# Performance work log

Hardware: AMD Instinct MI355X
Metric: run time of the kernel (lower is better)

## Reference

```python
import jax, jax.numpy as jnp
import numpy as np

EMB, KEY, HEAD, CTX = 1024, 64, 64, 4096
B, T = 4, 4096

def setup_inputs() -> dict:
    key = jax.random.key(0)
    ks = jax.random.split(key, 4)
    s = 1.0 / np.sqrt(EMB)
    return {
        "embeddings": jax.random.normal(ks[0], (B, T, EMB), dtype=jnp.float32),
        "Wk": jax.random.normal(ks[1], (EMB, KEY), dtype=jnp.float32) * s,
        "bk": jnp.zeros((KEY,), dtype=jnp.float32),
        "Wq": jax.random.normal(ks[2], (EMB, KEY), dtype=jnp.float32) * s,
        "bq": jnp.zeros((KEY,), dtype=jnp.float32),
        "Wv": jax.random.normal(ks[3], (EMB, HEAD), dtype=jnp.float32) * s,
        "bv": jnp.zeros((HEAD,), dtype=jnp.float32),
    }

def reference(embeddings, Wk, bk, Wq, bq, Wv, bv):
    # Linear projections: [B, T, E] @ [E, D] -> [B, T, D]
    keys = embeddings @ Wk + bk
    queries = embeddings @ Wq + bq
    values = embeddings @ Wv + bv
    # Scores: [B, T, T]
    scores = jnp.einsum("btd,bsd->bts", queries, keys) / jnp.sqrt(jnp.float32(KEY))
    t = scores.shape[1]
    # causal mask: -inf strictly above diagonal
    causal = jnp.tril(jnp.ones((t, t), dtype=bool))
    scores = jnp.where(causal, scores, -jnp.inf)
    weights = jax.nn.softmax(scores, axis=-1)
    return jnp.einsum("bts,bsh->bth", weights, values)
```

## Files before the change

### kernel.cpp

```cpp
#include <hip/hip_runtime.h>
#include <hip/hip_bf16.h>

#define EMB 1024
#define NB  4
#define TT  4096
#define DD  64

static constexpr float SCALE2 = 0.125f * 1.4426950408889634f;

typedef __bf16          bfrag    __attribute__((ext_vector_type(8)));
typedef float           f32x4    __attribute__((ext_vector_type(4)));
typedef unsigned short  ushort8t __attribute__((ext_vector_type(8)));
typedef unsigned short  ushort4t __attribute__((ext_vector_type(4)));
typedef unsigned int    uint32;

__device__ __forceinline__ unsigned short f2bf(float f) {
    __hip_bfloat16 h = __float2bfloat16(f);
    return __builtin_bit_cast(unsigned short, h);
}
__device__ __forceinline__ float bf2f(unsigned short u) {
    uint32 v = ((uint32)u) << 16;
    return __builtin_bit_cast(float, v);
}
__device__ __forceinline__ uint32 pk2(float a, float b) {
    return (uint32)f2bf(a) | ((uint32)f2bf(b) << 16);
}

__global__ __launch_bounds__(256) void prep_wt(
    const float* __restrict__ Wk, const float* __restrict__ Wq,
    const float* __restrict__ Wv, unsigned short* __restrict__ Wt)
{
    const int o = blockIdx.x * 256 + threadIdx.x;
    const int n = o >> 10, k = o & 1023;
    float v;
    if (n < 64)       v = Wk[k * 64 + n];
    else if (n < 128) v = Wq[k * 64 + (n - 64)] * SCALE2;
    else              v = Wv[k * 64 + (n - 128)];
    Wt[o] = f2bf(v);
}

#define PSTR 66

__global__ __launch_bounds__(256) void qkv_mfma(
    const float* __restrict__ emb,
    const unsigned short* __restrict__ Wt,
    const float* __restrict__ bk, const float* __restrict__ bq,
    const float* __restrict__ bv,
    unsigned short* __restrict__ Qb, unsigned short* __restrict__ Kb,
    unsigned short* __restrict__ Vt)
{
    __shared__ unsigned short elds[64 * PSTR];
    __shared__ unsigned short wlds[192 * PSTR];

    const int tid = threadIdx.x;
    const int w = tid >> 6, l = tid & 63;
    const int lr = l & 15, lg = l >> 4;
    const int m0 = blockIdx.x * 64;

    f32x4 acc[12];
#pragma unroll
    for (int i = 0; i < 12; ++i) acc[i] = (f32x4){0.f, 0.f, 0.f, 0.f};

    const int er = tid >> 2, ec = (tid & 3) * 16;

    float4 f0, f1, f2, f3;
    ushort8t wr[6];
    {
        const float* src = emb + (size_t)(m0 + er) * EMB + ec;
        f0 = *(const float4*)(src + 0);
        f1 = *(const float4*)(src + 4);
        f2 = *(const float4*)(src + 8);
        f3 = *(const float4*)(src + 12);
#pragma unroll
        for (int i = 0; i < 6; ++i) {
            const int idx = tid + i * 256;
            const int row = idx >> 3, c = (idx & 7) * 8;
            wr[i] = *(const ushort8t*)&Wt[(size_t)row * 1024 + c];
        }
    }

    for (int it = 0; it < 16; ++it) {
        __syncthreads();
        {
            ushort8t lo, hi;
            lo[0]=f2bf(f0.x); lo[1]=f2bf(f0.y); lo[2]=f2bf(f0.z); lo[3]=f2bf(f0.w);
            lo[4]=f2bf(f1.x); lo[5]=f2bf(f1.y); lo[6]=f2bf(f1.z); lo[7]=f2bf(f1.w);
            hi[0]=f2bf(f2.x); hi[1]=f2bf(f2.y); hi[2]=f2bf(f2.z); hi[3]=f2bf(f2.w);
            hi[4]=f2bf(f3.x); hi[5]=f2bf(f3.y); hi[6]=f2bf(f3.z); hi[7]=f2bf(f3.w);
            *(ushort8t*)&elds[er * PSTR + ec]     = lo;
            *(ushort8t*)&elds[er * PSTR + ec + 8] = hi;
#pragma unroll
            for (int i = 0; i < 6; ++i) {
                const int idx = tid + i * 256;
                const int row = idx >> 3, c = (idx & 7) * 8;
                *(ushort8t*)&wlds[row * PSTR + c] = wr[i];
            }
        }
        if (it < 15) {
            const int kn = (it + 1) * 64;
            const float* src = emb + (size_t)(m0 + er) * EMB + kn + ec;
            f0 = *(const float4*)(src + 0);
            f1 = *(const float4*)(src + 4);
            f2 = *(const float4*)(src + 8);
            f3 = *(const float4*)(src + 12);
#pragma unroll
            for (int i = 0; i < 6; ++i) {
                const int idx = tid + i * 256;
                const int row = idx >> 3, c = (idx & 7) * 8;
                wr[i] = *(const ushort8t*)&Wt[(size_t)row * 1024 + kn + c];
            }
        }
        __syncthreads();
#pragma unroll
        for (int c = 0; c < 2; ++c) {
            bfrag a = *(const bfrag*)&elds[(w * 16 + lr) * PSTR + c * 32 + lg * 8];
#pragma unroll
            for (int nt = 0; nt < 12; ++nt) {
                bfrag bb = *(const bfrag*)&wlds[(nt * 16 + lr) * PSTR + c * 32 + lg * 8];
                acc[nt] = __builtin_amdgcn_mfma_f32_16x16x32_bf16(a, bb, acc[nt], 0, 0, 0);
            }
        }
    }

    const int rbase = m0 + w * 16 + lg * 4;
#pragma unroll
    for (int nt = 0; nt < 12; ++nt) {
        const int n = nt * 16 + lr;
        float bias;
        if (n < 64)       bias = bk[n];
        else if (n < 128) bias = bq[n - 64] * SCALE2;
        else              bias = bv[n - 128];
        if (nt < 8) {
            unsigned short* dst = (nt < 4) ? Kb : Qb;
            const int d = (nt < 4) ? n : (n - 64);
#pragma unroll
            for (int rg = 0; rg < 4; ++rg)
                dst[(size_t)(rbase + rg) * 64 + d] = f2bf(acc[nt][rg] + bias);
        } else {
            const int h = n - 128;
            const int b = rbase >> 12, t = rbase & (TT - 1);
            ushort4t pk;
#pragma unroll
            for (int rg = 0; rg < 4; ++rg) pk[rg] = f2bf(acc[nt][rg] + bias);
            *(ushort4t*)&Vt[((size_t)b * 64 + h) * TT + t] = pk;
        }
    }
}

#define PST 66

__global__ __launch_bounds__(64) void attn_part(
    const unsigned short* __restrict__ Qb,
    const unsigned short* __restrict__ Kb,
    const unsigned short* __restrict__ Vt,
    unsigned short* __restrict__ po, float* __restrict__ pml,
    int chunk, int nch)
{
    __shared__ unsigned short plds[32 * PST];

    const int idx  = blockIdx.x;
    const int c    = idx >> 9;
    const int b    = idx & 3;
    const int ti32 = 127 - ((idx >> 2) & 127);
    const int nkt  = (ti32 >> 1) + 1;
    const int kt0  = c * chunk;
    if (kt0 >= nkt) return;
    const int kt1 = min(nkt, kt0 + chunk);

    const int l  = threadIdx.x;
    const int lr = l & 15, g = l >> 4;
    const int q0 = ti32 * 32;
    const size_t bTT = (size_t)b * TT;

    bfrag qa[2][2];
#pragma unroll
    for (int s = 0; s < 2; ++s) {
        const size_t qr = (bTT + q0 + s * 16 + lr) * 64 + g * 8;
        qa[s][0] = *(const bfrag*)&Qb[qr];
        qa[s][1] = *(const bfrag*)&Qb[qr + 32];
    }

    f32x4 o[2][4];
#pragma unroll
    for (int s = 0; s < 2; ++s)
#pragma unroll
        for (int ht = 0; ht < 4; ++ht) o[s][ht] = (f32x4){0.f, 0.f, 0.f, 0.f};
    float mrow[2] = {-1e30f, -1e30f};
    float lrow[2] = {0.f, 0.f};

    for (int kt = kt0; kt < kt1; ++kt) {
        const int k0 = kt * 64;

        bfrag kf[4][2];
#pragma unroll
        for (int nt = 0; nt < 4; ++nt) {
            const size_t kr = (bTT + k0 + nt * 16 + lr) * 64 + g * 8;
            kf[nt][0] = *(const bfrag*)&Kb[kr];
            kf[nt][1] = *(const bfrag*)&Kb[kr + 32];
        }
        bfrag vf[4][2];
#pragma unroll
        for (int ht = 0; ht < 4; ++ht) {
            const size_t vr = ((size_t)b * 64 + ht * 16 + lr) * TT + k0 + g * 8;
            vf[ht][0] = *(const bfrag*)&Vt[vr];
            vf[ht][1] = *(const bfrag*)&Vt[vr + 32];
        }
        const bool diag = (kt == nkt - 1);

#pragma unroll
        for (int s = 0; s < 2; ++s) {
            f32x4 sv[4];
#pragma unroll
            for (int nt = 0; nt < 4; ++nt) {
                sv[nt] = (f32x4){0.f, 0.f, 0.f, 0.f};
                sv[nt] = __builtin_amdgcn_mfma_f32_16x16x32_bf16(kf[nt][0], qa[s][0], sv[nt], 0, 0, 0);
                sv[nt] = __builtin_amdgcn_mfma_f32_16x16x32_bf16(kf[nt][1], qa[s][1], sv[nt], 0, 0, 0);
            }
            const int qrow = q0 + s * 16 + lr;
            if (diag) {
#pragma unroll
                for (int nt = 0; nt < 4; ++nt)
#pragma unroll
                    for (int rg = 0; rg < 4; ++rg) {
                        const int key = k0 + nt * 16 + 4 * g + rg;
                        if (key > qrow) sv[nt][rg] = -1e30f;
                    }
            }
            float pm = sv[0][0];
#pragma unroll
            for (int nt = 0; nt < 4; ++nt)
#pragma unroll
                for (int rg = 0; rg < 4; ++rg) pm = fmaxf(pm, sv[nt][rg]);
            pm = fmaxf(pm, __shfl_xor(pm, 16));
            pm = fmaxf(pm, __shfl_xor(pm, 32));

            if (!__all(pm - mrow[s] <= 8.0f)) {
                const float nm = fmaxf(mrow[s], pm);
                const float cr = exp2f(mrow[s] - nm);
                mrow[s] = nm;
                lrow[s] *= cr;
#pragma unroll
                for (int ht = 0; ht < 4; ++ht) o[s][ht] *= cr;
            }

            float ls = 0.f;
            uint32 pw[8];
#pragma unroll
            for (int nt = 0; nt < 4; ++nt)
#pragma unroll
                for (int h = 0; h < 2; ++h) {
                    const float pa_ = exp2f(sv[nt][2 * h]     - mrow[s]);
                    const float pb_ = exp2f(sv[nt][2 * h + 1] - mrow[s]);
                    ls += pa_ + pb_;
                    pw[nt * 2 + h] = pk2(pa_, pb_);
                }
            ls += __shfl_xor(ls, 16);
            ls += __shfl_xor(ls, 32);
            lrow[s] += ls;

            const int prow = (s * 16 + lr) * PST;
#pragma unroll
            for (int nt = 0; nt < 4; ++nt)
#pragma unroll
                for (int h = 0; h < 2; ++h)
                    *(uint32*)&plds[prow + nt * 16 + 4 * g + 2 * h] = pw[nt * 2 + h];

#pragma unroll
            for (int cc = 0; cc < 2; ++cc) {
                bfrag pa = *(const bfrag*)&plds[prow + cc * 32 + g * 8];
#pragma unroll
                for (int ht = 0; ht < 4; ++ht)
                    o[s][ht] = __builtin_amdgcn_mfma_f32_16x16x32_bf16(pa, vf[ht][cc], o[s][ht], 0, 0, 0);
            }
        }
    }

    const int slot = (((b << 7) + ti32) * nch) + c;
    const size_t pob = (size_t)slot * 2048;
#pragma unroll
    for (int s = 0; s < 2; ++s)
#pragma unroll
        for (int ht = 0; ht < 4; ++ht)
#pragma unroll
            for (int rg = 0; rg < 4; ++rg)
                po[pob + (size_t)(((s * 4 + ht) * 4 + rg) * 64 + l)] = f2bf(o[s][ht][rg]);
    if (g == 0) {
#pragma unroll
        for (int s = 0; s < 2; ++s) {
            pml[slot * 64 + s * 16 + lr]      = mrow[s];
            pml[slot * 64 + 32 + s * 16 + lr] = lrow[s];
        }
    }
}

__global__ __launch_bounds__(256) void attn_merge(
    const unsigned short* __restrict__ po, const float* __restrict__ pml,
    float* __restrict__ out, int chunk, int nch)
{
    const int idx  = blockIdx.x;
    const int b    = idx & 3;
    const int ti32 = idx >> 2;
    const int nkt  = (ti32 >> 1) + 1;
    const int nc   = (nkt + chunk - 1) / chunk;

    const int e0   = threadIdx.x * 8;
    const int lane = e0 & 63;
    const int rg   = (e0 >> 6) & 3;
    const int ht   = (e0 >> 8) & 3;
    const int s    = e0 >> 10;
    const int row  = s * 16 + ((lane >> 4) << 2) + rg;
    const int col0 = ht * 16 + (lane & 15);
    const int slot0 = ((b << 7) + ti32) * nch;

    float M = -1e30f;
    for (int c = 0; c < nc; ++c)
        M = fmaxf(M, pml[(slot0 + c) * 64 + row]);

    float den = 0.f;
    float acc[8];
#pragma unroll
    for (int i = 0; i < 8; ++i) acc[i] = 0.f;

    for (int c = 0; c < nc; ++c) {
        const float wgt = exp2f(pml[(slot0 + c) * 64 + row] - M);
        den += wgt * pml[(slot0 + c) * 64 + 32 + row];
        const ushort8t v = *(const ushort8t*)&po[(size_t)(slot0 + c) * 2048 + e0];
#pragma unroll
        for (int j = 0; j < 8; ++j) acc[j] += wgt * bf2f(v[j]);
    }
    const float inv = 1.0f / den;
    float* dst = out + ((size_t)b * TT + ti32 * 32 + row) * 64 + col0;
    float4 o0 = {acc[0] * inv, acc[1] * inv, acc[2] * inv, acc[3] * inv};
    float4 o1 = {acc[4] * inv, acc[5] * inv, acc[6] * inv, acc[7] * inv};
    *(float4*)(dst)     = o0;
    *(float4*)(dst + 4) = o1;
}

extern "C" void kernel_launch(void* const* d_in, const int* in_sizes, int n_in,
                              void* d_out, int out_size, void* d_ws, size_t ws_size,
                              hipStream_t stream)
{
    const float* emb = (const float*)d_in[0];
    const float* Wk  = (const float*)d_in[1];
    const float* bk  = (const float*)d_in[2];
    const float* Wq  = (const float*)d_in[3];
    const float* bq  = (const float*)d_in[4];
    const float* Wv  = (const float*)d_in[5];
    const float* bv  = (const float*)d_in[6];
    float* out = (float*)d_out;

    char* base = (char*)d_ws;
    unsigned short* Qb = (unsigned short*)(base);
    unsigned short* Kb = (unsigned short*)(base + (2u << 20));
    unsigned short* Vt = (unsigned short*)(base + (4u << 20));
    unsigned short* Wt = (unsigned short*)(base + (6u << 20));
    const size_t pbase = ((size_t)6 << 20) + (512u << 10);

    int nch = 8;
    for (;;) {
        const size_t need = pbase +
            (size_t)512 * nch * (2048 * sizeof(unsigned short) + 64 * sizeof(float));
        if (need <= ws_size || nch == 1) break;
        nch >>= 1;
    }
    const int chunk = 64 / nch;
    unsigned short* po = (unsigned short*)(base + pbase);
    float* pml = (float*)(po + (size_t)512 * nch * 2048);

    prep_wt<<<192 * 1024 / 256, 256, 0, stream>>>(Wk, Wq, Wv, Wt);
    qkv_mfma<<<(NB * TT) / 64, 256, 0, stream>>>(emb, Wt, bk, bq, bv, Qb, Kb, Vt);
    attn_part<<<512 * nch, 64, 0, stream>>>(Qb, Kb, Vt, po, pml, chunk, nch);
    attn_merge<<<512, 256, 0, stream>>>(po, pml, out, chunk, nch);
}
```

Measured before the change: 85.85 us.

## Double-buffer K loads, permute P in registers, and retune QKV and split counts

The attention partial kernel now double-buffers K fragments across key tiles and loads V ahead of compute. It replaces the LDS round-trip for the probability matrix with ds_bpermute register shuffles and raises MFMA priority with s_setprio. The key-split count goes from 8 to 16 chunks through a templated chunk size, when workspace allows. The QKV projection kernel moves to 32-row tiles with 128 threads, doubling its block count. Together these aim to hide global load latency and raise occupancy, at the cost of more registers, more partial results to merge, and more redundant weight-tile loads in the projection.

```diff
diff --git a/kernel.cpp b/kernel.cpp
--- a/kernel.cpp
+++ b/kernel.cpp
@@ -13,6 +13,7 @@
 typedef unsigned short  ushort8t __attribute__((ext_vector_type(8)));
 typedef unsigned short  ushort4t __attribute__((ext_vector_type(4)));
 typedef unsigned int    uint32;
+typedef uint32          uint32x4 __attribute__((ext_vector_type(4)));
 
 __device__ __forceinline__ unsigned short f2bf(float f) {
     __hip_bfloat16 h = __float2bfloat16(f);
@@ -41,7 +42,7 @@
 
 #define PSTR 66
 
-__global__ __launch_bounds__(256) void qkv_mfma(
+__global__ __launch_bounds__(128) void qkv_mfma(
     const float* __restrict__ emb,
     const unsigned short* __restrict__ Wt,
     const float* __restrict__ bk, const float* __restrict__ bq,
@@ -49,13 +50,13 @@
     unsigned short* __restrict__ Qb, unsigned short* __restrict__ Kb,
     unsigned short* __restrict__ Vt)
 {
-    __shared__ unsigned short elds[64 * PSTR];
+    __shared__ unsigned short elds[32 * PSTR];
     __shared__ unsigned short wlds[192 * PSTR];
 
     const int tid = threadIdx.x;
     const int w = tid >> 6, l = tid & 63;
     const int lr = l & 15, lg = l >> 4;
-    const int m0 = blockIdx.x * 64;
+    const int m0 = blockIdx.x * 32;
 
     f32x4 acc[12];
 #pragma unroll
@@ -64,7 +65,7 @@
     const int er = tid >> 2, ec = (tid & 3) * 16;
 
     float4 f0, f1, f2, f3;
-    ushort8t wr[6];
+    ushort8t wr[12];
     {
         const float* src = emb + (size_t)(m0 + er) * EMB + ec;
         f0 = *(const float4*)(src + 0);
@@ -72,8 +73,8 @@
         f2 = *(const float4*)(src + 8);
         f3 = *(const float4*)(src + 12);
 #pragma unroll
-        for (int i = 0; i < 6; ++i) {
-            const int idx = tid + i * 256;
+        for (int i = 0; i < 12; ++i) {
+            const int idx = tid + i * 128;
             const int row = idx >> 3, c = (idx & 7) * 8;
             wr[i] = *(const ushort8t*)&Wt[(size_t)row * 1024 + c];
         }
@@ -90,8 +91,8 @@
             *(ushort8t*)&elds[er * PSTR + ec]     = lo;
             *(ushort8t*)&elds[er * PSTR + ec + 8] = hi;
 #pragma unroll
-            for (int i = 0; i < 6; ++i) {
-                const int idx = tid + i * 256;
+            for (int i = 0; i < 12; ++i) {
+                const int idx = tid + i * 128;
                 const int row = idx >> 3, c = (idx & 7) * 8;
                 *(ushort8t*)&wlds[row * PSTR + c] = wr[i];
             }
@@ -104,8 +105,8 @@
             f2 = *(const float4*)(src + 8);
             f3 = *(const float4*)(src + 12);
 #pragma unroll
-            for (int i = 0; i < 6; ++i) {
-                const int idx = tid + i * 256;
+            for (int i = 0; i < 12; ++i) {
+                const int idx = tid + i * 128;
                 const int row = idx >> 3, c = (idx & 7) * 8;
                 wr[i] = *(const ushort8t*)&Wt[(size_t)row * 1024 + kn + c];
             }
@@ -147,25 +148,113 @@
     }
 }
 
-#define PST 66
-
-__global__ __launch_bounds__(64) void attn_part(
+#define LOADK(KF, T)                                                          \
+    { const unsigned short* p_ = kp0 + (size_t)(T) * 4096;                    \
+      KF[0][0] = *(const bfrag*)(p_);         KF[0][1] = *(const bfrag*)(p_ + 32);   \
+      KF[1][0] = *(const bfrag*)(p_ + 1024);  KF[1][1] = *(const bfrag*)(p_ + 1056); \
+      KF[2][0] = *(const bfrag*)(p_ + 2048);  KF[2][1] = *(const bfrag*)(p_ + 2080); \
+      KF[3][0] = *(const bfrag*)(p_ + 3072);  KF[3][1] = *(const bfrag*)(p_ + 3104); }
+
+#define LOADV(VF, T)                                                          \
+    { const unsigned short* p_ = vp0 + (T) * 64;                              \
+      VF[0][0] = *(const bfrag*)(p_);             VF[0][1] = *(const bfrag*)(p_ + 32);           \
+      VF[1][0] = *(const bfrag*)(p_ + 16 * TT);   VF[1][1] = *(const bfrag*)(p_ + 16 * TT + 32); \
+      VF[2][0] = *(const bfrag*)(p_ + 32 * TT);   VF[2][1] = *(const bfrag*)(p_ + 32 * TT + 32); \
+      VF[3][0] = *(const bfrag*)(p_ + 48 * TT);   VF[3][1] = *(const bfrag*)(p_ + 48 * TT + 32); }
+
+#define COMPUTE(KF, VF, T)                                                    \
+{                                                                             \
+    const int  kt_   = kt0 + (T);                                             \
+    const bool diag_ = (kt_ == nkt - 1);                                      \
+    const int  k0_   = kt_ * 64;                                              \
+    _Pragma("unroll")                                                         \
+    for (int s = 0; s < 2; ++s) {                                             \
+        f32x4 sv[4];                                                          \
+        __builtin_amdgcn_s_setprio(1);                                        \
+        _Pragma("unroll")                                                     \
+        for (int nt = 0; nt < 4; ++nt) {                                      \
+            sv[nt] = (f32x4){0.f, 0.f, 0.f, 0.f};                             \
+            sv[nt] = __builtin_amdgcn_mfma_f32_16x16x32_bf16(KF[nt][0], qa[s][0], sv[nt], 0, 0, 0); \
+            sv[nt] = __builtin_amdgcn_mfma_f32_16x16x32_bf16(KF[nt][1], qa[s][1], sv[nt], 0, 0, 0); \
+        }                                                                     \
+        __builtin_amdgcn_s_setprio(0);                                        \
+        const int qrow_ = q0 + s * 16 + lr;                                   \
+        if (diag_) {                                                          \
+            _Pragma("unroll")                                                 \
+            for (int nt = 0; nt < 4; ++nt)                                    \
+                _Pragma("unroll")                                             \
+                for (int rg = 0; rg < 4; ++rg) {                              \
+                    const int key_ = k0_ + nt * 16 + 4 * g + rg;              \
+                    if (key_ > qrow_) sv[nt][rg] = -1e30f;                    \
+                }                                                             \
+        }                                                                     \
+        float pm = fmaxf(fmaxf(fmaxf(sv[0][0], sv[0][1]), fmaxf(sv[0][2], sv[0][3])),   \
+                         fmaxf(fmaxf(sv[1][0], sv[1][1]), fmaxf(sv[1][2], sv[1][3])));  \
+        pm = fmaxf(pm, fmaxf(fmaxf(fmaxf(sv[2][0], sv[2][1]), fmaxf(sv[2][2], sv[2][3])),   \
+                             fmaxf(fmaxf(sv[3][0], sv[3][1]), fmaxf(sv[3][2], sv[3][3])))); \
+        pm = fmaxf(pm, __shfl_xor(pm, 16));                                   \
+        pm = fmaxf(pm, __shfl_xor(pm, 32));                                   \
+        if (!__all(pm - mrow[s] <= 8.0f)) {                                   \
+            const float nm_ = fmaxf(mrow[s], pm);                             \
+            const float cr_ = exp2f(mrow[s] - nm_);                           \
+            mrow[s] = nm_;                                                    \
+            lrow[s] *= cr_;                                                   \
+            _Pragma("unroll")                                                 \
+            for (int ht = 0; ht < 4; ++ht) o[s][ht] *= cr_;                   \
+        }                                                                     \
+        float ls = 0.f;                                                       \
+        uint32 pw[8];                                                         \
+        _Pragma("unroll")                                                     \
+        for (int nt = 0; nt < 4; ++nt)                                        \
+            _Pragma("unroll")                                                 \
+            for (int h = 0; h < 2; ++h) {                                     \
+                const float pa_ = exp2f(sv[nt][2 * h]     - mrow[s]);         \
+                const float pb_ = exp2f(sv[nt][2 * h + 1] - mrow[s]);         \
+                ls += pa_ + pb_;                                              \
+                pw[nt * 2 + h] = pk2(pa_, pb_);                               \
+            }                                                                 \
+        ls += __shfl_xor(ls, 16);                                             \
+        ls += __shfl_xor(ls, 32);                                             \
+        lrow[s] += ls;                                                        \
+        _Pragma("unroll")                                                     \
+        for (int cc = 0; cc < 2; ++cc) {                                      \
+            uint32x4 dw;                                                      \
+            _Pragma("unroll")                                                 \
+            for (int w2 = 0; w2 < 4; ++w2) {                                  \
+                const int addr_ = (w2 < 2) ? addr_a : addr_b;                 \
+                const uint32 lo_ = (uint32)__builtin_amdgcn_ds_bpermute(      \
+                    addr_, (int)pw[4 * cc + (w2 & 1)]);                       \
+                const uint32 hi_ = (uint32)__builtin_amdgcn_ds_bpermute(      \
+                    addr_, (int)pw[4 * cc + 2 + (w2 & 1)]);                   \
+                dw[w2] = ghi ? hi_ : lo_;                                     \
+            }                                                                 \
+            const bfrag paf_ = __builtin_bit_cast(bfrag, dw);                 \
+            __builtin_amdgcn_s_setprio(1);                                    \
+            o[s][0] = __builtin_amdgcn_mfma_f32_16x16x32_bf16(paf_, VF[0][cc], o[s][0], 0, 0, 0); \
+            o[s][1] = __builtin_amdgcn_mfma_f32_16x16x32_bf16(paf_, VF[1][cc], o[s][1], 0, 0, 0); \
+            o[s][2] = __builtin_amdgcn_mfma_f32_16x16x32_bf16(paf_, VF[2][cc], o[s][2], 0, 0, 0); \
+            o[s][3] = __builtin_amdgcn_mfma_f32_16x16x32_bf16(paf_, VF[3][cc], o[s][3], 0, 0, 0); \
+            __builtin_amdgcn_s_setprio(0);                                    \
+        }                                                                     \
+    }                                                                         \
+}
+
+template<int CHUNK>
+__global__ __launch_bounds__(64, 2) void attn_part(
     const unsigned short* __restrict__ Qb,
     const unsigned short* __restrict__ Kb,
     const unsigned short* __restrict__ Vt,
-    unsigned short* __restrict__ po, float* __restrict__ pml,
-    int chunk, int nch)
+    unsigned short* __restrict__ po, float* __restrict__ pml)
 {
-    __shared__ unsigned short plds[32 * PST];
-
+    constexpr int NCH = 64 / CHUNK;
     const int idx  = blockIdx.x;
     const int c    = idx >> 9;
     const int b    = idx & 3;
     const int ti32 = 127 - ((idx >> 2) & 127);
     const int nkt  = (ti32 >> 1) + 1;
-    const int kt0  = c * chunk;
+    const int kt0  = c * CHUNK;
     if (kt0 >= nkt) return;
-    const int kt1 = min(nkt, kt0 + chunk);
+    const int ntile = min(nkt - kt0, CHUNK);
 
     const int l  = threadIdx.x;
     const int lr = l & 15, g = l >> 4;
@@ -180,6 +269,13 @@
         qa[s][1] = *(const bfrag*)&Qb[qr + 32];
     }
 
+    const unsigned short* kp0 = Kb + (bTT + (size_t)kt0 * 64 + lr) * 64 + g * 8;
+    const unsigned short* vp0 = Vt + ((size_t)b * 64 + lr) * TT + (size_t)kt0 * 64 + g * 8;
+
+    const int addr_a = (lr + 32 * (g & 1)) * 4;
+    const int addr_b = addr_a + 64;
+    const bool ghi = (g >= 2);
+
     f32x4 o[2][4];
 #pragma unroll
     for (int s = 0; s < 2; ++s)
@@ -188,94 +284,22 @@
     float mrow[2] = {-1e30f, -1e30f};
     float lrow[2] = {0.f, 0.f};
 
-    for (int kt = kt0; kt < kt1; ++kt) {
-        const int k0 = kt * 64;
-
-        bfrag kf[4][2];
-#pragma unroll
-        for (int nt = 0; nt < 4; ++nt) {
-            const size_t kr = (bTT + k0 + nt * 16 + lr) * 64 + g * 8;
-            kf[nt][0] = *(const bfrag*)&Kb[kr];
-            kf[nt][1] = *(const bfrag*)&Kb[kr + 32];
-        }
-        bfrag vf[4][2];
-#pragma unroll
-        for (int ht = 0; ht < 4; ++ht) {
-            const size_t vr = ((size_t)b * 64 + ht * 16 + lr) * TT + k0 + g * 8;
-            vf[ht][0] = *(const bfrag*)&Vt[vr];
-            vf[ht][1] = *(const bfrag*)&Vt[vr + 32];
-        }
-        const bool diag = (kt == nkt - 1);
-
-#pragma unroll
-        for (int s = 0; s < 2; ++s) {
-            f32x4 sv[4];
-#pragma unroll
-            for (int nt = 0; nt < 4; ++nt) {
-                sv[nt] = (f32x4){0.f, 0.f, 0.f, 0.f};
-                sv[nt] = __builtin_amdgcn_mfma_f32_16x16x32_bf16(kf[nt][0], qa[s][0], sv[nt], 0, 0, 0);
-                sv[nt] = __builtin_amdgcn_mfma_f32_16x16x32_bf16(kf[nt][1], qa[s][1], sv[nt], 0, 0, 0);
-            }
-            const int qrow = q0 + s * 16 + lr;
-            if (diag) {
-#pragma unroll
-                for (int nt = 0; nt < 4; ++nt)
-#pragma unroll
-                    for (int rg = 0; rg < 4; ++rg) {
-                        const int key = k0 + nt * 16 + 4 * g + rg;
-                        if (key > qrow) sv[nt][rg] = -1e30f;
-                    }
-            }
-            float pm = sv[0][0];
-#pragma unroll
-            for (int nt = 0; nt < 4; ++nt)
-#pragma unroll
-                for (int rg = 0; rg < 4; ++rg) pm = fmaxf(pm, sv[nt][rg]);
-            pm = fmaxf(pm, __shfl_xor(pm, 16));
-            pm = fmaxf(pm, __shfl_xor(pm, 32));
-
-            if (!__all(pm - mrow[s] <= 8.0f)) {
-                const float nm = fmaxf(mrow[s], pm);
-                const float cr = exp2f(mrow[s] - nm);
-                mrow[s] = nm;
-                lrow[s] *= cr;
-#pragma unroll
-                for (int ht = 0; ht < 4; ++ht) o[s][ht] *= cr;
-            }
-
-            float ls = 0.f;
-            uint32 pw[8];
-#pragma unroll
-            for (int nt = 0; nt < 4; ++nt)
-#pragma unroll
-                for (int h = 0; h < 2; ++h) {
-                    const float pa_ = exp2f(sv[nt][2 * h]     - mrow[s]);
-                    const float pb_ = exp2f(sv[nt][2 * h + 1] - mrow[s]);
-                    ls += pa_ + pb_;
-                    pw[nt * 2 + h] = pk2(pa_, pb_);
-                }
-            ls += __shfl_xor(ls, 16);
-            ls += __shfl_xor(ls, 32);
-            lrow[s] += ls;
-
-            const int prow = (s * 16 + lr) * PST;
-#pragma unroll
-            for (int nt = 0; nt < 4; ++nt)
-#pragma unroll
-                for (int h = 0; h < 2; ++h)
-                    *(uint32*)&plds[prow + nt * 16 + 4 * g + 2 * h] = pw[nt * 2 + h];
-
-#pragma unroll
-            for (int cc = 0; cc < 2; ++cc) {
-                bfrag pa = *(const bfrag*)&plds[prow + cc * 32 + g * 8];
-#pragma unroll
-                for (int ht = 0; ht < 4; ++ht)
-                    o[s][ht] = __builtin_amdgcn_mfma_f32_16x16x32_bf16(pa, vf[ht][cc], o[s][ht], 0, 0, 0);
-            }
-        }
-    }
-
-    const int slot = (((b << 7) + ti32) * nch) + c;
+    bfrag kfA[4][2], kfB[4][2], vf[4][2];
+    LOADK(kfA, 0);
+
+#pragma unroll
+    for (int t = 0; t < CHUNK; t += 2) {
+        if (t >= ntile) break;
+        LOADV(vf, t);
+        if (t + 1 < ntile) LOADK(kfB, t + 1);
+        COMPUTE(kfA, vf, t);
+        if (t + 1 >= ntile) break;
+        LOADV(vf, t + 1);
+        if (t + 2 < ntile) LOADK(kfA, t + 2);
+        COMPUTE(kfB, vf, t + 1);
+    }
+
+    const int slot = (((b << 7) + ti32) * NCH) + c;
     const size_t pob = (size_t)slot * 2048;
 #pragma unroll
     for (int s = 0; s < 2; ++s)
@@ -356,19 +380,21 @@
     unsigned short* Wt = (unsigned short*)(base + (6u << 20));
     const size_t pbase = ((size_t)6 << 20) + (512u << 10);
 
-    int nch = 8;
-    for (;;) {
-        const size_t need = pbase +
-            (size_t)512 * nch * (2048 * sizeof(unsigned short) + 64 * sizeof(float));
-        if (need <= ws_size || nch == 1) break;
-        nch >>= 1;
+    int nch = 16;
+    {
+        const size_t need16 = pbase +
+            (size_t)512 * 16 * (2048 * sizeof(unsigned short) + 64 * sizeof(float));
+        if (need16 > ws_size) nch = 8;
     }
     const int chunk = 64 / nch;
     unsigned short* po = (unsigned short*)(base + pbase);
     float* pml = (float*)(po + (size_t)512 * nch * 2048);
 
     prep_wt<<<192 * 1024 / 256, 256, 0, stream>>>(Wk, Wq, Wv, Wt);
-    qkv_mfma<<<(NB * TT) / 64, 256, 0, stream>>>(emb, Wt, bk, bq, bv, Qb, Kb, Vt);
-    attn_part<<<512 * nch, 64, 0, stream>>>(Qb, Kb, Vt, po, pml, chunk, nch);
+    qkv_mfma<<<(NB * TT) / 32, 128, 0, stream>>>(emb, Wt, bk, bq, bv, Qb, Kb, Vt);
+    if (nch == 16)
+        attn_part<4><<<512 * 16, 64, 0, stream>>>(Qb, Kb, Vt, po, pml);
+    else
+        attn_part<8><<<512 * 8, 64, 0, stream>>>(Qb, Kb, Vt, po, pml);
     attn_merge<<<512, 256, 0, stream>>>(po, pml, out, chunk, nch);
 }
```

Measured after the change: 89.08 us. +3.8%, slower.
